# Kernel optimization log

Measured on AMD Instinct MI355X. Metric: run time of the kernel, lower is better.

The kernel has to match this reference:

```python
import jax, jax.numpy as jnp
import numpy as np

N_NODES = 100000
N_EDGES = 1600000
HID = 128


def setup_inputs() -> dict:
    key = jax.random.key(0)
    k1, k2, k3, k4, k5 = jax.random.split(key, 5)
    node_embeddings = jax.random.normal(k1, (N_NODES, HID), dtype=jnp.float32)
    src_idx = jax.random.randint(k2, (N_EDGES,), 0, N_NODES, dtype=jnp.int64)
    tgt_idx = jax.random.randint(k3, (N_EDGES,), 0, N_NODES, dtype=jnp.int64)
    # Params of the selected edge-type predictor (Linear(2h,h) -> ReLU -> Linear(h,1))
    W1 = jax.random.normal(k4, (2 * HID, HID), dtype=jnp.float32) * (1.0 / np.sqrt(2 * HID))
    b1 = jnp.zeros((HID,), dtype=jnp.float32)
    W2 = jax.random.normal(k5, (HID, 1), dtype=jnp.float32) * (1.0 / np.sqrt(HID))
    b2 = jnp.zeros((1,), dtype=jnp.float32)
    return {
        "node_embeddings": node_embeddings,
        "src_idx": src_idx,
        "tgt_idx": tgt_idx,
        "edge_type_idx": 0,
        "W1": W1,
        "b1": b1,
        "W2": W2,
        "b2": b2,
    }


def reference(node_embeddings, src_idx, tgt_idx, edge_type_idx, W1, b1, W2, b2):
    # edge_type_idx selects a predictor; params passed in are that predictor's.
    src_emb = node_embeddings[src_idx]  # [E, H]
    tgt_emb = node_embeddings[tgt_idx]  # [E, H]
    # cat([src,tgt]) @ W1 == src @ W1[:H] + tgt @ W1[H:]  (avoids materializing pair_feat)
    h = jax.nn.relu(src_emb @ W1[:HID] + tgt_emb @ W1[HID:] + b1)  # [E, H]
    out = h @ W2 + b2  # [E, 1]
    return out[:, 0]  # squeeze(-1) -> [E]
```

## Files before the change

kernel.cpp:

```cpp
#include <hip/hip_runtime.h>
#include <hip/hip_bf16.h>

#define HID 128

typedef __attribute__((ext_vector_type(8))) short short8;
typedef __attribute__((ext_vector_type(4))) float f32x4;
typedef __attribute__((ext_vector_type(16))) float f32x16;
typedef __attribute__((ext_vector_type(4))) unsigned int u32x4;
typedef __attribute__((ext_vector_type(2))) _Float16 h2;

__device__ __forceinline__ short f2bf(float x) {
    __bf16 b = (__bf16)x;
    return __builtin_bit_cast(short, b);
}


__global__ __launch_bounds__(256) void hist_pack_kernel(
    const float* __restrict__ W1, short* __restrict__ bpk2,
    const void* __restrict__ src_raw, const void* __restrict__ tgt_raw,
    int E, float bscale, int* __restrict__ gh)
{
    const int tid = threadIdx.x;

    if (blockIdx.x < 16) {
        int t = blockIdx.x * 256 + tid;
        int l    = t & 63;
        int ks   = (t >> 6) & 7;
        int nt   = (t >> 9) & 3;
        int half = t >> 11;
        int k0  = half * 128 + ks * 16 + (l >> 5) * 8;
        int col = nt * 32 + (l & 31);
        short8 v;
#pragma unroll
        for (int j = 0; j < 8; ++j)
            v[j] = f2bf(W1[(k0 + j) * HID + col]);
        *reinterpret_cast<short8*>(&bpk2[t * 8]) = v;
    }

    __shared__ int lh[64];
    if (tid < 64) lh[tid] = 0;
    __syncthreads();

    int i64f = 1;
    {
        const int* s32 = (const int*)src_raw;
#pragma unroll
        for (int i = 1; i < 32; i += 2) i64f &= (s32[i] == 0);
    }
    const int stride = gridDim.x * 256;
    for (int e = blockIdx.x * 256 + tid; e < E; e += stride) {
        int t = i64f ? (int)((const long long*)tgt_raw)[e]
                     : ((const int*)tgt_raw)[e];
        int b = (int)((float)t * bscale);
        b = b < 0 ? 0 : (b > 63 ? 63 : b);
        atomicAdd(&lh[b], 1);
    }
    __syncthreads();
    if (tid < 64 && lh[tid]) atomicAdd(&gh[tid], lh[tid]);
}

__global__ __launch_bounds__(512, 4) void uv_kernel(
    const float* __restrict__ emb,
    const short* __restrict__ bpk2,
    unsigned short* __restrict__ U,
    unsigned short* __restrict__ V,
    int Nn)
{
    __shared__ short lds_b[32768];

    const int tid = threadIdx.x;
    const int l   = tid & 63;
    const int wid = tid >> 6;
    const int wg  = wid >> 1;
    const int wn  = wid & 1;
    const int lc  = l & 31;
    const int hi  = l >> 5;

    {
        const u32x4* g = (const u32x4*)bpk2;
        u32x4* d = (u32x4*)lds_b;
#pragma unroll
        for (int i = 0; i < 8; ++i) d[i * 512 + tid] = g[i * 512 + tid];
    }
    __syncthreads();

    const int base = blockIdx.x * 128 + wg * 32;
    int nr = base + lc;
    if (nr >= Nn) nr = Nn - 1;

    f32x16 accU[2], accV[2];
#pragma unroll
    for (int n = 0; n < 2; ++n) { accU[n] = (f32x16)(0.f); accV[n] = (f32x16)(0.f); }

#pragma unroll
    for (int ks = 0; ks < 8; ++ks) {
        const float* p = emb + (size_t)nr * HID + ks * 16 + hi * 8;
        f32x4 x0 = *reinterpret_cast<const f32x4*>(p);
        f32x4 x1 = *reinterpret_cast<const f32x4*>(p + 4);
        short8 afr;
#pragma unroll
        for (int j = 0; j < 4; ++j) { afr[j] = f2bf(x0[j]); afr[4 + j] = f2bf(x1[j]); }
#pragma unroll
        for (int n = 0; n < 2; ++n) {
            const int nt = wn * 2 + n;
            short8 bU = *reinterpret_cast<const short8*>(&lds_b[(((0 + nt) * 8 + ks) * 64 + l) * 8]);
            short8 bV = *reinterpret_cast<const short8*>(&lds_b[(((4 + nt) * 8 + ks) * 64 + l) * 8]);
            accU[n] = __builtin_amdgcn_mfma_f32_32x32x16_bf16(afr, bU, accU[n], 0, 0, 0);
            accV[n] = __builtin_amdgcn_mfma_f32_32x32x16_bf16(afr, bV, accV[n], 0, 0, 0);
        }
    }

#pragma unroll
    for (int n = 0; n < 2; ++n) {
        const int col = wn * 64 + n * 32 + lc;
#pragma unroll
        for (int r = 0; r < 16; ++r) {
            const int row = (r & 3) + 8 * (r >> 2) + 4 * hi;
            const int node = base + row;
            if (node < Nn) {
                _Float16 hu = (_Float16)accU[n][r];
                _Float16 hv = (_Float16)accV[n][r];
                U[(size_t)node * HID + col] = __builtin_bit_cast(unsigned short, hu);
                V[(size_t)node * HID + col] = __builtin_bit_cast(unsigned short, hv);
            }
        }
    }
}

__global__ __launch_bounds__(256) void scatter64_kernel(
    const void* __restrict__ src_raw, const void* __restrict__ tgt_raw,
    int E, float bscale,
    const int* __restrict__ gh, int* __restrict__ cursor,
    unsigned long long* __restrict__ rec)
{
    __shared__ int lh[64], lh2[64], lo[64], grb[64], go[64];
    __shared__ unsigned long long sR[2048];

    const int tid = threadIdx.x;
    int i64f = 1;
    {
        const int* s32 = (const int*)src_raw;
#pragma unroll
        for (int i = 1; i < 32; i += 2) i64f &= (s32[i] == 0);
    }
    if (tid < 64) { lh[tid] = 0; lh2[tid] = 0; }
    __syncthreads();

    const int base = blockIdx.x * 2048;
    int myS[8], myT[8], myB[8];
#pragma unroll
    for (int k = 0; k < 8; ++k) {
        const int e = base + k * 256 + tid;
        myB[k] = -1;
        if (e < E) {
            int s, t;
            if (i64f) {
                s = (int)((const long long*)src_raw)[e];
                t = (int)((const long long*)tgt_raw)[e];
            } else {
                s = ((const int*)src_raw)[e];
                t = ((const int*)tgt_raw)[e];
            }
            int b = (int)((float)t * bscale);
            b = b < 0 ? 0 : (b > 63 ? 63 : b);
            myS[k] = s; myT[k] = t; myB[k] = b;
            atomicAdd(&lh[b], 1);
        }
    }
    __syncthreads();
    if (tid < 64) {
        int vl = lh[tid], vg = gh[tid];
        int il = vl, ig = vg;
#pragma unroll
        for (int off = 1; off < 64; off <<= 1) {
            int xl = __shfl_up(il, off, 64);
            int xg = __shfl_up(ig, off, 64);
            if (tid >= off) { il += xl; ig += xg; }
        }
        lo[tid] = il - vl;
        go[tid] = ig - vg;
        grb[tid] = (vl > 0) ? atomicAdd(&cursor[tid], vl) : 0;
    }
    __syncthreads();
#pragma unroll
    for (int k = 0; k < 8; ++k) {
        if (myB[k] >= 0) {
            const int b = myB[k];
            const int pl = lo[b] + atomicAdd(&lh2[b], 1);
            sR[pl] = (unsigned long long)(unsigned)(base + k * 256 + tid)
                   | ((unsigned long long)(unsigned)myS[k] << 21)
                   | ((unsigned long long)(unsigned)myT[k] << 38);
        }
    }
    __syncthreads();
    const int total = lo[63] + lh[63];
    for (int i = tid; i < total; i += 256) {
        const unsigned long long r = sR[i];
        const int t = (int)(r >> 38);
        int b = (int)((float)t * bscale);
        b = b < 0 ? 0 : (b > 63 ? 63 : b);
        rec[go[b] + grb[b] + (i - lo[b])] = r;
    }
}

__global__ __launch_bounds__(256) void edge_pass_part_kernel(
    const unsigned short* __restrict__ U,
    const unsigned short* __restrict__ V,
    const unsigned long long* __restrict__ rec,
    const int* __restrict__ gh,
    const float* __restrict__ b1,
    const float* __restrict__ W2,
    const float* __restrict__ b2,
    float* __restrict__ out,
    int per_x)
{
    __shared__ int sh_off8[9];

    const int tid = threadIdx.x;
    if (tid < 64) {
        int v = gh[tid];
        int inc = v;
#pragma unroll
        for (int off = 1; off < 64; off <<= 1) {
            int x = __shfl_up(inc, off, 64);
            if (tid >= off) inc += x;
        }
        if ((tid & 7) == 0) sh_off8[tid >> 3] = inc - v;
        if (tid == 63) sh_off8[8] = inc;
    }
    __syncthreads();

    const int l   = tid & 63;
    const int wid = tid >> 6;
    const int le  = l >> 4;
    const int lc  = l & 15;
    const int p   = blockIdx.x & 7;
    const int r   = blockIdx.x >> 3;

    const int pbeg = sh_off8[p];
    const int pend = sh_off8[p + 1];

    h2 b1p[4], w2p[4];
    {
        f32x4 a = *reinterpret_cast<const f32x4*>(b1 + lc * 8);
        f32x4 b = *reinterpret_cast<const f32x4*>(b1 + lc * 8 + 4);
        f32x4 c = *reinterpret_cast<const f32x4*>(W2 + lc * 8);
        f32x4 d = *reinterpret_cast<const f32x4*>(W2 + lc * 8 + 4);
#pragma unroll
        for (int j = 0; j < 2; ++j) {
            b1p[0][j] = (_Float16)a[j];     b1p[1][j] = (_Float16)a[2 + j];
            b1p[2][j] = (_Float16)b[j];     b1p[3][j] = (_Float16)b[2 + j];
            w2p[0][j] = (_Float16)c[j];     w2p[1][j] = (_Float16)c[2 + j];
            w2p[2][j] = (_Float16)d[j];     w2p[3][j] = (_Float16)d[2 + j];
        }
    }
    const float b2s = b2[0];
    const h2 zero2 = (h2)((_Float16)0.f);

    for (int base = pbeg + r * 64; base < pend; base += per_x * 64) {
        short8 ub[4], vb[4];
        int oid[4];
        bool live[4];
#pragma unroll
        for (int g = 0; g < 4; ++g) {
            int pos = base + wid * 16 + g * 4 + le;
            live[g] = (pos < pend);
            if (!live[g]) pos = base;
            const unsigned long long rc = rec[pos];
            oid[g] = (int)(rc & 0x1FFFFF);
            const unsigned s = (unsigned)((rc >> 21) & 0x1FFFF);
            const unsigned t = (unsigned)(rc >> 38);
            ub[g] = *reinterpret_cast<const short8*>(U + s * HID + lc * 8);
            vb[g] = *reinterpret_cast<const short8*>(V + t * HID + lc * 8);
        }

#pragma unroll
        for (int g = 0; g < 4; ++g) {
            const unsigned int* uw = (const unsigned int*)&ub[g];
            const unsigned int* vw = (const unsigned int*)&vb[g];
            h2 s2 = zero2;
#pragma unroll
            for (int j = 0; j < 4; ++j) {
                h2 hu = __builtin_bit_cast(h2, uw[j]);
                h2 hv = __builtin_bit_cast(h2, vw[j]);
                h2 h  = hu + hv + b1p[j];
                h = __builtin_elementwise_max(h, zero2);
                s2 = s2 + h * w2p[j];
            }
            float s = (float)s2[0] + (float)s2[1];
#pragma unroll
            for (int w = 1; w < 16; w <<= 1)
                s += __shfl_xor(s, w, 16);
            if (lc == 0 && live[g])
                out[oid[g]] = s + b2s;
        }
    }
}

__global__ __launch_bounds__(256) void edge_pass_kernel(
    const unsigned short* __restrict__ U,
    const unsigned short* __restrict__ V,
    const void* __restrict__ src_raw,
    const void* __restrict__ tgt_raw,
    const float* __restrict__ b1,
    const float* __restrict__ W2,
    const float* __restrict__ b2,
    float* __restrict__ out,
    int E)
{
    const int tid = threadIdx.x;
    const int l   = tid & 63;
    const int wid = tid >> 6;
    const int le  = l >> 4;
    const int lc  = l & 15;

    int oddw = 0;
    {
        const int* s32 = (const int*)src_raw;
        if (l < 32) oddw = s32[2 * l + 1];
    }
    const bool i64f = (__ballot(oddw != 0) == 0ULL);

    h2 b1p[4], w2p[4];
    {
        f32x4 a = *reinterpret_cast<const f32x4*>(b1 + lc * 8);
        f32x4 b = *reinterpret_cast<const f32x4*>(b1 + lc * 8 + 4);
        f32x4 c = *reinterpret_cast<const f32x4*>(W2 + lc * 8);
        f32x4 d = *reinterpret_cast<const f32x4*>(W2 + lc * 8 + 4);
#pragma unroll
        for (int j = 0; j < 2; ++j) {
            b1p[0][j] = (_Float16)a[j];     b1p[1][j] = (_Float16)a[2 + j];
            b1p[2][j] = (_Float16)b[j];     b1p[3][j] = (_Float16)b[2 + j];
            w2p[0][j] = (_Float16)c[j];     w2p[1][j] = (_Float16)c[2 + j];
            w2p[2][j] = (_Float16)d[j];     w2p[3][j] = (_Float16)d[2 + j];
        }
    }
    const float b2s = b2[0];
    const h2 zero2 = (h2)((_Float16)0.f);

    const long long ebase = ((long long)blockIdx.x * 4 + wid) * 16;

    short8 ub[4], vb[4];
#pragma unroll
    for (int g = 0; g < 4; ++g) {
        long long e = ebase + g * 4 + le;
        if (e >= E) e = E - 1;
        long long si, ti;
        if (i64f) {
            si = ((const long long*)src_raw)[e];
            ti = ((const long long*)tgt_raw)[e];
        } else {
            si = ((const int*)src_raw)[e];
            ti = ((const int*)tgt_raw)[e];
        }
        ub[g] = *reinterpret_cast<const short8*>(U + (unsigned)si * HID + lc * 8);
        vb[g] = *reinterpret_cast<const short8*>(V + (unsigned)ti * HID + lc * 8);
    }

#pragma unroll
    for (int g = 0; g < 4; ++g) {
        const unsigned int* uw = (const unsigned int*)&ub[g];
        const unsigned int* vw = (const unsigned int*)&vb[g];
        h2 s2 = zero2;
#pragma unroll
        for (int j = 0; j < 4; ++j) {
            h2 hu = __builtin_bit_cast(h2, uw[j]);
            h2 hv = __builtin_bit_cast(h2, vw[j]);
            h2 h  = hu + hv + b1p[j];
            h = __builtin_elementwise_max(h, zero2);
            s2 = s2 + h * w2p[j];
        }
        float s = (float)s2[0] + (float)s2[1];
#pragma unroll
        for (int w = 1; w < 16; w <<= 1)
            s += __shfl_xor(s, w, 16);
        const long long e = ebase + g * 4 + le;
        if (lc == 0 && e < E)
            out[e] = s + b2s;
    }
}


__global__ void pack_w1_kernel(const float* __restrict__ W1, short* __restrict__ bpk) {
    int t = blockIdx.x * 256 + threadIdx.x;
    int f = (t >> 6) & 7;
    int l = t & 63;
    int n = t >> 9;
    int c = l & 15, kb = l >> 4;
    int k0 = f * 32 + kb * 8;
    short8 v;
#pragma unroll
    for (int j = 0; j < 8; ++j)
        v[j] = f2bf(W1[(k0 + j) * HID + n * 16 + c]);
    *reinterpret_cast<short8*>(&bpk[t * 8]) = v;
}

__global__ __launch_bounds__(256) void conv_emb_kernel(
    const float* __restrict__ emb, short* __restrict__ bemb, int n8) {
    int i = blockIdx.x * 256 + threadIdx.x;
    if (i >= n8) return;
    f32x4 x0 = *reinterpret_cast<const f32x4*>(emb + (size_t)i * 8);
    f32x4 x1 = *reinterpret_cast<const f32x4*>(emb + (size_t)i * 8 + 4);
    short8 v;
#pragma unroll
    for (int j = 0; j < 4; ++j) {
        v[j]     = f2bf(x0[j]);
        v[4 + j] = f2bf(x1[j]);
    }
    *reinterpret_cast<short8*>(&bemb[(size_t)i * 8]) = v;
}

template <int MODE>
__global__ __launch_bounds__(512, 4) void edge_head_kernel(
    const float* __restrict__ emb,
    const short* __restrict__ bemb,
    const void* __restrict__ src_raw,
    const void* __restrict__ tgt_raw,
    const float* __restrict__ W1,
    const float* __restrict__ b1,
    const float* __restrict__ W2,
    const float* __restrict__ b2,
    const short* __restrict__ bpk,
    float* __restrict__ out,
    int E)
{
    __shared__ short lds_b[32768];

    const int tid = threadIdx.x;

    int i64f = 1;
    {
        const int* s32 = (const int*)src_raw;
#pragma unroll
        for (int i = 1; i < 32; i += 2) i64f &= (s32[i] == 0);
    }

    if (MODE != 2) {
        const u32x4* g = (const u32x4*)bpk;
        u32x4* d = (u32x4*)lds_b;
#pragma unroll
        for (int i = 0; i < 8; ++i) d[i * 512 + tid] = g[i * 512 + tid];
    } else {
        for (int i = 0; i < 64; ++i) {
            int idx = i * 512 + tid;
            int col = idx & 127;
            int k   = idx >> 7;
            int n = col >> 4, cc = col & 15;
            int f = k >> 5, kb = (k >> 3) & 3, j = k & 7;
            int l2 = kb * 16 + cc;
            lds_b[(((n * 8 + f) * 64 + l2) << 3) + j] = f2bf(W1[idx]);
        }
    }
    __syncthreads();

    const int l = tid & 63;
    const int wid = tid >> 6;
    const int c = l & 15;
    const int g = l >> 4;
    const long long e0 = (long long)blockIdx.x * 256 + wid * 32;

    unsigned so[2], to[2];
#pragma unroll
    for (int m = 0; m < 2; ++m) {
        long long e = e0 + m * 16 + c;
        if (e >= E) e = E - 1;
        long long si, ti;
        if (i64f) {
            si = ((const long long*)src_raw)[e];
            ti = ((const long long*)tgt_raw)[e];
        } else {
            si = ((const int*)src_raw)[e];
            ti = ((const int*)tgt_raw)[e];
        }
        so[m] = (unsigned)si * HID;
        to[m] = (unsigned)ti * HID;
    }

    f32x4 acc[2][8];
#pragma unroll
    for (int m = 0; m < 2; ++m)
#pragma unroll
        for (int n = 0; n < 8; ++n)
            acc[m][n] = (f32x4){0.f, 0.f, 0.f, 0.f};

    const int koff = g * 8;
#pragma unroll
    for (int f = 0; f < 8; ++f) {
        short8 afr[2];
        const int k0 = (f & 3) * 32 + koff;
#pragma unroll
        for (int m = 0; m < 2; ++m) {
            const unsigned off = (f < 4 ? so[m] : to[m]) + k0;
            if (MODE == 0) {
                afr[m] = *reinterpret_cast<const short8*>(bemb + off);
            } else {
                f32x4 x0 = *reinterpret_cast<const f32x4*>(emb + off);
                f32x4 x1 = *reinterpret_cast<const f32x4*>(emb + off + 4);
                short8 t;
#pragma unroll
                for (int j = 0; j < 4; ++j) {
                    t[j]     = f2bf(x0[j]);
                    t[4 + j] = f2bf(x1[j]);
                }
                afr[m] = t;
            }
        }
#pragma unroll
        for (int n = 0; n < 8; ++n) {
            short8 bfr = *reinterpret_cast<const short8*>(&lds_b[((n * 8 + f) * 64 + l) * 8]);
#pragma unroll
            for (int m = 0; m < 2; ++m)
                acc[m][n] = __builtin_amdgcn_mfma_f32_16x16x32_bf16(afr[m], bfr, acc[m][n], 0, 0, 0);
        }
    }

    float b1v[8], w2v[8];
#pragma unroll
    for (int n = 0; n < 8; ++n) {
        b1v[n] = b1[n * 16 + c];
        w2v[n] = W2[n * 16 + c];
    }
    const float b2s = b2[0];

#pragma unroll
    for (int m = 0; m < 2; ++m) {
        float s[4] = {0.f, 0.f, 0.f, 0.f};
#pragma unroll
        for (int n = 0; n < 8; ++n) {
#pragma unroll
            for (int r = 0; r < 4; ++r)
                s[r] += fmaxf(acc[m][n][r] + b1v[n], 0.f) * w2v[n];
        }
#pragma unroll
        for (int w = 1; w < 16; w <<= 1) {
#pragma unroll
            for (int r = 0; r < 4; ++r)
                s[r] += __shfl_xor(s[r], w, 16);
        }
        if (c == 0) {
            const long long eb = e0 + m * 16 + g * 4;
#pragma unroll
            for (int r = 0; r < 4; ++r)
                if (eb + r < E) out[eb + r] = s[r] + b2s;
        }
    }
}

extern "C" void kernel_launch(void* const* d_in, const int* in_sizes, int n_in,
                              void* d_out, int out_size, void* d_ws, size_t ws_size,
                              hipStream_t stream) {
    const float* emb = (const float*)d_in[0];
    const void*  src = d_in[1];
    const void*  tgt = d_in[2];
    const float* W1 = (const float*)d_in[4];
    const float* b1 = (const float*)d_in[5];
    const float* W2 = (const float*)d_in[6];
    const float* b2 = (const float*)d_in[7];
    float* out = (float*)d_out;

    const int E  = in_sizes[1];
    const int Nn = in_sizes[0] / HID;

    const size_t uv_bytes = (size_t)Nn * HID * sizeof(short);
    const size_t off_gh   = 65536;
    const size_t off_U    = 65536 + 4096;
    const size_t off_V    = off_U + uv_bytes;
    const size_t off_rec  = off_V + uv_bytes;
    const size_t need_part = off_rec + (size_t)E * 8;
    const size_t need_uv   = 65536 + 2 * uv_bytes;
    const size_t need_old  = 65536 + (size_t)in_sizes[0] * sizeof(short);

    const bool packable = (Nn <= (1 << 17)) && (E <= (1 << 21));

    if (ws_size >= need_part && E >= 4096 && packable) {
        short*              bpk2   = (short*)d_ws;
        int*                gh     = (int*)((char*)d_ws + off_gh);
        int*                cursor = gh + 64;
        unsigned short*     U      = (unsigned short*)((char*)d_ws + off_U);
        unsigned short*     Vv     = (unsigned short*)((char*)d_ws + off_V);
        unsigned long long* rec    = (unsigned long long*)((char*)d_ws + off_rec);

        const float bscale = 63.9999f / (float)Nn;

        hipMemsetAsync(gh, 0, 512, stream);
        hist_pack_kernel<<<256, 256, 0, stream>>>(W1, bpk2, src, tgt, E, bscale, gh);
        uv_kernel<<<(Nn + 127) / 128, 512, 0, stream>>>(emb, bpk2, U, Vv, Nn);
        scatter64_kernel<<<(E + 2047) / 2048, 256, 0, stream>>>(
            src, tgt, E, bscale, gh, cursor, rec);
        const int per_x = (E / 8 + 4096) / 64 + 2;
        edge_pass_part_kernel<<<per_x * 8, 256, 0, stream>>>(
            U, Vv, rec, gh, b1, W2, b2, out, per_x);
        return;
    }

    if (ws_size >= need_uv) {
        short*          bpk2 = (short*)d_ws;
        unsigned short* U    = (unsigned short*)((char*)d_ws + 65536);
        unsigned short* Vv   = (unsigned short*)((char*)d_ws + 65536 + uv_bytes);

        hist_pack_kernel<<<16, 256, 0, stream>>>(W1, bpk2, src, tgt, 0, 1.0f, nullptr);
        uv_kernel<<<(Nn + 127) / 128, 512, 0, stream>>>(emb, bpk2, U, Vv, Nn);
        edge_pass_kernel<<<(E + 63) / 64, 256, 0, stream>>>(U, Vv, src, tgt, b1, W2, b2, out, E);
        return;
    }

    short* bpk  = (short*)d_ws;
    short* bemb = (short*)((char*)d_ws + 65536);

    int mode;
    if (ws_size >= need_old)        mode = 0;
    else if (ws_size >= 65536)      mode = 1;
    else                            mode = 2;

    if (mode != 2)
        pack_w1_kernel<<<16, 256, 0, stream>>>(W1, bpk);
    if (mode == 0) {
        const int n8 = in_sizes[0] / 8;
        conv_emb_kernel<<<(n8 + 255) / 256, 256, 0, stream>>>(emb, bemb, n8);
    }

    const int grid = (E + 255) / 256;
    if (mode == 0)
        edge_head_kernel<0><<<grid, 512, 0, stream>>>(emb, bemb, src, tgt, W1, b1, W2, b2, bpk, out, E);
    else if (mode == 1)
        edge_head_kernel<1><<<grid, 512, 0, stream>>>(emb, bemb, src, tgt, W1, b1, W2, b2, bpk, out, E);
    else
        edge_head_kernel<2><<<grid, 512, 0, stream>>>(emb, bemb, src, tgt, W1, b1, W2, b2, bpk, out, E);
}
```

Before: 145.2 us.

## Coarsen edge bucketing to 8 bins with ballot-based scatter and larger edge tiles

The target-node bucketing drops from 64 to 8 bins. The scatter kernel now ranks edges with wave ballots and popcounts and writes records straight to global memory, replacing LDS atomics and a staged shared-memory reorder. The edge pass handles 128 edges per block iteration with 8 gathers in flight per thread, and the grid size is adjusted to match. This removes LDS atomic contention and a sync/copy stage in the scatter, but the coarser bins give weaker target locality, and the per-wave direct writes are less coalesced.

```diff
diff --git a/kernel.cpp b/kernel.cpp
--- a/kernel.cpp
+++ b/kernel.cpp
@@ -37,8 +37,8 @@
         *reinterpret_cast<short8*>(&bpk2[t * 8]) = v;
     }
 
-    __shared__ int lh[64];
-    if (tid < 64) lh[tid] = 0;
+    __shared__ int lh[8];
+    if (tid < 8) lh[tid] = 0;
     __syncthreads();
 
     int i64f = 1;
@@ -52,11 +52,11 @@
         int t = i64f ? (int)((const long long*)tgt_raw)[e]
                      : ((const int*)tgt_raw)[e];
         int b = (int)((float)t * bscale);
-        b = b < 0 ? 0 : (b > 63 ? 63 : b);
+        b = b < 0 ? 0 : (b > 7 ? 7 : b);
         atomicAdd(&lh[b], 1);
     }
     __syncthreads();
-    if (tid < 64 && lh[tid]) atomicAdd(&gh[tid], lh[tid]);
+    if (tid < 8 && lh[tid]) atomicAdd(&gh[tid], lh[tid]);
 }
 
 __global__ __launch_bounds__(512, 4) void uv_kernel(
@@ -127,24 +127,38 @@
     }
 }
 
-__global__ __launch_bounds__(256) void scatter64_kernel(
+__global__ __launch_bounds__(256) void scatter8_kernel(
     const void* __restrict__ src_raw, const void* __restrict__ tgt_raw,
     int E, float bscale,
     const int* __restrict__ gh, int* __restrict__ cursor,
     unsigned long long* __restrict__ rec)
 {
-    __shared__ int lh[64], lh2[64], lo[64], grb[64], go[64];
-    __shared__ unsigned long long sR[2048];
+    __shared__ int wcnt_lds[4][8];
+    __shared__ int lo[4][8];
+    __shared__ int grb[8];
+    __shared__ int go[8];
 
     const int tid = threadIdx.x;
+    const int l   = tid & 63;
+    const int w   = tid >> 6;
+
     int i64f = 1;
     {
         const int* s32 = (const int*)src_raw;
 #pragma unroll
         for (int i = 1; i < 32; i += 2) i64f &= (s32[i] == 0);
     }
-    if (tid < 64) { lh[tid] = 0; lh2[tid] = 0; }
-    __syncthreads();
+
+    if (tid < 8) {
+        int v = gh[tid];
+        int inc = v;
+#pragma unroll
+        for (int off = 1; off < 8; off <<= 1) {
+            int x = __shfl_up(inc, off, 8);
+            if (tid >= off) inc += x;
+        }
+        go[tid] = inc - v;
+    }
 
     const int base = blockIdx.x * 2048;
     int myS[8], myT[8], myB[8];
@@ -162,44 +176,57 @@
                 t = ((const int*)tgt_raw)[e];
             }
             int b = (int)((float)t * bscale);
-            b = b < 0 ? 0 : (b > 63 ? 63 : b);
+            b = b < 0 ? 0 : (b > 7 ? 7 : b);
             myS[k] = s; myT[k] = t; myB[k] = b;
-            atomicAdd(&lh[b], 1);
-        }
-    }
+        }
+    }
+
+    int wcnt[8];
+#pragma unroll
+    for (int b = 0; b < 8; ++b) wcnt[b] = 0;
+#pragma unroll
+    for (int k = 0; k < 8; ++k) {
+#pragma unroll
+        for (int b = 0; b < 8; ++b) {
+            unsigned long long m = __ballot(myB[k] == b);
+            wcnt[b] += (int)__popcll(m);
+        }
+    }
+    if (l < 8) wcnt_lds[w][l] = wcnt[l];
     __syncthreads();
-    if (tid < 64) {
-        int vl = lh[tid], vg = gh[tid];
-        int il = vl, ig = vg;
-#pragma unroll
-        for (int off = 1; off < 64; off <<= 1) {
-            int xl = __shfl_up(il, off, 64);
-            int xg = __shfl_up(ig, off, 64);
-            if (tid >= off) { il += xl; ig += xg; }
-        }
-        lo[tid] = il - vl;
-        go[tid] = ig - vg;
-        grb[tid] = (vl > 0) ? atomicAdd(&cursor[tid], vl) : 0;
+
+    if (tid < 8) {
+        const int c0 = wcnt_lds[0][tid];
+        const int c1 = wcnt_lds[1][tid];
+        const int c2 = wcnt_lds[2][tid];
+        const int c3 = wcnt_lds[3][tid];
+        lo[0][tid] = 0;
+        lo[1][tid] = c0;
+        lo[2][tid] = c0 + c1;
+        lo[3][tid] = c0 + c1 + c2;
+        const int bc = c0 + c1 + c2 + c3;
+        grb[tid] = (bc > 0) ? atomicAdd(&cursor[tid], bc) : 0;
     }
     __syncthreads();
+
+    const unsigned long long ltmask = (l == 63) ? (~0ull >> 1) : ((1ull << l) - 1);
+    int wrun[8];
+#pragma unroll
+    for (int b = 0; b < 8; ++b) wrun[b] = 0;
 #pragma unroll
     for (int k = 0; k < 8; ++k) {
-        if (myB[k] >= 0) {
-            const int b = myB[k];
-            const int pl = lo[b] + atomicAdd(&lh2[b], 1);
-            sR[pl] = (unsigned long long)(unsigned)(base + k * 256 + tid)
-                   | ((unsigned long long)(unsigned)myS[k] << 21)
-                   | ((unsigned long long)(unsigned)myT[k] << 38);
-        }
-    }
-    __syncthreads();
-    const int total = lo[63] + lh[63];
-    for (int i = tid; i < total; i += 256) {
-        const unsigned long long r = sR[i];
-        const int t = (int)(r >> 38);
-        int b = (int)((float)t * bscale);
-        b = b < 0 ? 0 : (b > 63 ? 63 : b);
-        rec[go[b] + grb[b] + (i - lo[b])] = r;
+#pragma unroll
+        for (int b = 0; b < 8; ++b) {
+            unsigned long long m = __ballot(myB[k] == b);
+            if (myB[k] == b) {
+                const int rank = (int)__popcll(m & ltmask);
+                const int pos = go[b] + grb[b] + lo[w][b] + wrun[b] + rank;
+                rec[pos] = (unsigned long long)(unsigned)(base + k * 256 + tid)
+                         | ((unsigned long long)(unsigned)myS[k] << 21)
+                         | ((unsigned long long)(unsigned)myT[k] << 38);
+            }
+            wrun[b] += (int)__popcll(m);
+        }
     }
 }
 
@@ -214,19 +241,19 @@
     float* __restrict__ out,
     int per_x)
 {
-    __shared__ int sh_off8[9];
+    __shared__ int sh_off[9];
 
     const int tid = threadIdx.x;
-    if (tid < 64) {
+    if (tid < 8) {
         int v = gh[tid];
         int inc = v;
 #pragma unroll
-        for (int off = 1; off < 64; off <<= 1) {
-            int x = __shfl_up(inc, off, 64);
+        for (int off = 1; off < 8; off <<= 1) {
+            int x = __shfl_up(inc, off, 8);
             if (tid >= off) inc += x;
         }
-        if ((tid & 7) == 0) sh_off8[tid >> 3] = inc - v;
-        if (tid == 63) sh_off8[8] = inc;
+        sh_off[tid] = inc - v;
+        if (tid == 7) sh_off[8] = inc;
     }
     __syncthreads();
 
@@ -237,8 +264,8 @@
     const int p   = blockIdx.x & 7;
     const int r   = blockIdx.x >> 3;
 
-    const int pbeg = sh_off8[p];
-    const int pend = sh_off8[p + 1];
+    const int pbeg = sh_off[p];
+    const int pend = sh_off[p + 1];
 
     h2 b1p[4], w2p[4];
     {
@@ -257,13 +284,13 @@
     const float b2s = b2[0];
     const h2 zero2 = (h2)((_Float16)0.f);
 
-    for (int base = pbeg + r * 64; base < pend; base += per_x * 64) {
-        short8 ub[4], vb[4];
-        int oid[4];
-        bool live[4];
-#pragma unroll
-        for (int g = 0; g < 4; ++g) {
-            int pos = base + wid * 16 + g * 4 + le;
+    for (int base = pbeg + r * 128; base < pend; base += per_x * 128) {
+        short8 ub[8], vb[8];
+        int oid[8];
+        bool live[8];
+#pragma unroll
+        for (int g = 0; g < 8; ++g) {
+            int pos = base + wid * 32 + g * 4 + le;
             live[g] = (pos < pend);
             if (!live[g]) pos = base;
             const unsigned long long rc = rec[pos];
@@ -275,7 +302,7 @@
         }
 
 #pragma unroll
-        for (int g = 0; g < 4; ++g) {
+        for (int g = 0; g < 8; ++g) {
             const unsigned int* uw = (const unsigned int*)&ub[g];
             const unsigned int* vw = (const unsigned int*)&vb[g];
             h2 s2 = zero2;
@@ -575,19 +602,19 @@
     if (ws_size >= need_part && E >= 4096 && packable) {
         short*              bpk2   = (short*)d_ws;
         int*                gh     = (int*)((char*)d_ws + off_gh);
-        int*                cursor = gh + 64;
+        int*                cursor = gh + 8;
         unsigned short*     U      = (unsigned short*)((char*)d_ws + off_U);
         unsigned short*     Vv     = (unsigned short*)((char*)d_ws + off_V);
         unsigned long long* rec    = (unsigned long long*)((char*)d_ws + off_rec);
 
-        const float bscale = 63.9999f / (float)Nn;
-
-        hipMemsetAsync(gh, 0, 512, stream);
+        const float bscale = 7.9999f / (float)Nn;
+
+        hipMemsetAsync(gh, 0, 64, stream);
         hist_pack_kernel<<<256, 256, 0, stream>>>(W1, bpk2, src, tgt, E, bscale, gh);
         uv_kernel<<<(Nn + 127) / 128, 512, 0, stream>>>(emb, bpk2, U, Vv, Nn);
-        scatter64_kernel<<<(E + 2047) / 2048, 256, 0, stream>>>(
+        scatter8_kernel<<<(E + 2047) / 2048, 256, 0, stream>>>(
             src, tgt, E, bscale, gh, cursor, rec);
-        const int per_x = (E / 8 + 4096) / 64 + 2;
+        const int per_x = (E / 8 + 8192) / 128 + 1;
         edge_pass_part_kernel<<<per_x * 8, 256, 0, stream>>>(
             U, Vv, rec, gh, b1, W2, b2, out, per_x);
         return;
```

Result: slower. 159.5 us (+9.8%).
